# Performance work log

Measured on AMD Instinct MI355X. Metric: run time of the kernel, lower is better.

## Reference

```python
import jax, jax.numpy as jnp
import numpy as np

N_NODES = 100000
N_EDGES = 1600000
IN_F, H1, H2, H3, H4, H5, H6, NC = 512, 512, 256, 64, 64, 64, 64, 40


def _linear_params(key, fan_in, fan_out):
    k1, k2 = jax.random.split(key)
    bound = 1.0 / np.sqrt(fan_in)
    W = jax.random.uniform(k1, (fan_in, fan_out), minval=-bound, maxval=bound, dtype=jnp.float32)
    b = jax.random.uniform(k2, (fan_out,), minval=-bound, maxval=bound, dtype=jnp.float32)
    return W, b


def setup_inputs() -> dict:
    key = jax.random.key(0)
    ks = jax.random.split(key, 10)
    x = jax.random.normal(ks[0], (N_NODES, IN_F), dtype=jnp.float32)
    src = jax.random.randint(ks[1], (N_EDGES,), 0, N_NODES, dtype=jnp.int32)
    dst = jax.random.randint(ks[2], (N_EDGES,), 0, N_NODES, dtype=jnp.int32)
    W1, b1 = _linear_params(ks[3], IN_F, H1)
    W2, b2 = _linear_params(ks[4], H1, H2)
    W3, b3 = _linear_params(ks[5], H2, H3)
    Wg1, bg1 = _linear_params(ks[6], H3, H4)
    Wg2, bg2 = _linear_params(ks[7], H4, H5)
    Wg3, bg3 = _linear_params(ks[8], H5, H6)
    Wg4, bg4 = _linear_params(ks[9], H6, NC)
    return {"x": x, "src": src, "dst": dst,
            "W1": W1, "b1": b1, "W2": W2, "b2": b2, "W3": W3, "b3": b3,
            "Wg1": Wg1, "bg1": bg1, "Wg2": Wg2, "bg2": bg2,
            "Wg3": Wg3, "bg3": bg3, "Wg4": Wg4, "bg4": bg4}


def _graph_conv(h, src, dst, norm_src, norm_dst, W, b):
    # DGL GraphConv, norm='both': D_dst^{-1/2} A D_src^{-1/2} H W + b
    msg = (h * norm_src[:, None])[src]            # [E, d] gather from source nodes
    agg = jax.ops.segment_sum(msg, dst, num_segments=N_NODES)  # scatter-add to dst
    agg = agg * norm_dst[:, None]
    return agg @ W + b


def reference(x, src, dst, W1, b1, W2, b2, W3, b3,
              Wg1, bg1, Wg2, bg2, Wg3, bg3, Wg4, bg4):
    ones = jnp.ones((N_EDGES,), dtype=jnp.float32)
    deg_out = jax.ops.segment_sum(ones, src, num_segments=N_NODES)
    deg_in = jax.ops.segment_sum(ones, dst, num_segments=N_NODES)
    norm_src = jax.lax.rsqrt(jnp.clip(deg_out, 1.0))
    norm_dst = jax.lax.rsqrt(jnp.clip(deg_in, 1.0))

    h = jax.nn.relu(x @ W1 + b1)
    h = jax.nn.relu(h @ W2 + b2)
    h = jax.nn.relu(h @ W3 + b3)
    h = jax.nn.relu(_graph_conv(h, src, dst, norm_src, norm_dst, Wg1, bg1))
    h = jax.nn.relu(_graph_conv(h, src, dst, norm_src, norm_dst, Wg2, bg2))
    h = jax.nn.relu(_graph_conv(h, src, dst, norm_src, norm_dst, Wg3, bg3))
    h = jax.nn.relu(_graph_conv(h, src, dst, norm_src, norm_dst, Wg4, bg4))
    return h
```

## Files before the change

kernel.cpp:

```cpp
#include <hip/hip_runtime.h>

#define N_NODES 100000
#define N_EDGES 1600000
#define M_PAD   100096
#define BCAP    64
#define X_REAL 51200000L
#define X_PAD  ((long)M_PAD*512)

typedef __bf16 bf16x8 __attribute__((ext_vector_type(8)));
typedef float  f32x4  __attribute__((ext_vector_type(4)));
typedef unsigned short u16x8 __attribute__((ext_vector_type(8)));

__device__ __forceinline__ unsigned short f2bf(float f) {
  union { float f; unsigned u; } x; x.f = f;
  unsigned r = (x.u + 0x7FFFu + ((x.u >> 16) & 1u)) >> 16;
  return (unsigned short)r;
}

__device__ __forceinline__ void async_copy16(const void* g, void* l) {
  __builtin_amdgcn_global_load_lds((__attribute__((address_space(1))) void*)g,
                                   (__attribute__((address_space(3))) void*)l,
                                   16, 0, 0);
}


__global__ void cvt_x_kernel(const float* __restrict__ x, unsigned short* __restrict__ xb) {
  long e = ((long)blockIdx.x * 256 + threadIdx.x) * 8;
  u16x8 o;
  if (e < X_REAL) {
    float4 f0 = *(const float4*)(x + e);
    float4 f1 = *(const float4*)(x + e + 4);
    o[0] = f2bf(f0.x); o[1] = f2bf(f0.y); o[2] = f2bf(f0.z); o[3] = f2bf(f0.w);
    o[4] = f2bf(f1.x); o[5] = f2bf(f1.y); o[6] = f2bf(f1.z); o[7] = f2bf(f1.w);
  } else {
    o = (u16x8)0;
  }
  *(u16x8*)(xb + e) = o;
}

__global__ void cvt_wt_kernel(const float* __restrict__ W, unsigned short* __restrict__ Wt,
                              int K, int N, int Npad) {
  int idx = blockIdx.x * 256 + threadIdx.x;
  if (idx >= Npad * K) return;
  int n = idx / K, k = idx % K;
  Wt[idx] = (n < N) ? f2bf(W[(long)k * N + n]) : (unsigned short)0;
}

__global__ void norms_kernel(const int* __restrict__ hist,
                             float* __restrict__ nsrc, float* __restrict__ ndst) {
  int i = blockIdx.x * 256 + threadIdx.x;
  if (i >= M_PAD) return;
  if (i < N_NODES) {
    nsrc[i] = rsqrtf(fmaxf((float)hist[N_NODES + i], 1.f));
    ndst[i] = rsqrtf(fmaxf((float)hist[i], 1.f));
  } else {
    nsrc[i] = 1.f;
  }
}

template <int BM, int BN, int BK, int EPI, bool EDGES>
__launch_bounds__(256)
__global__ void gemm_bt(const unsigned short* __restrict__ A,
                        const unsigned short* __restrict__ Bt,
                        const float* __restrict__ bias,
                        const float* __restrict__ rowscale,
                        void* __restrict__ C, int K, int Nfull,
                        const int* __restrict__ esrc, const int* __restrict__ edst,
                        int* __restrict__ hist, int* __restrict__ bucket) {
  if constexpr (EDGES) {
    if (blockIdx.x == gridDim.x - 1) {
      const int stride = gridDim.y * 256;
      for (int e = blockIdx.y * 256 + threadIdx.x; e < N_EDGES; e += stride) {
        int s = esrc[e], d = edst[e];
        atomicAdd(&hist[N_NODES + s], 1);
        int p = atomicAdd(&hist[d], 1);
        if (p < BCAP) bucket[(size_t)d * BCAP + p] = s;
      }
      return;
    }
  }
  constexpr int WM = BM / 2, WN = BN / 2;
  constexpr int MI = WM / 16, NI = WN / 16;
  __shared__ __align__(16) unsigned short As[BM * BK];
  __shared__ __align__(16) unsigned short Bs[BN * BK];
  const int tid = threadIdx.x;
  const int wave = tid >> 6, lane = tid & 63;
  const int wm0 = (wave >> 1) * WM, wn0 = (wave & 1) * WN;
  const long rowBase = (long)blockIdx.y * BM;
  const int colBase = blockIdx.x * BN;
  const unsigned short* Ab = A + rowBase * K;
  const unsigned short* Bb = Bt + (long)colBase * K;
  f32x4 acc[MI][NI] = {};
  constexpr int ACH = BM * BK / 8;
  constexpr int BCH = BN * BK / 8;
  for (int k0 = 0; k0 < K; k0 += BK) {
#pragma unroll
    for (int c = tid; c < ACH; c += 256) {
      int r = (c * 8) / BK, cc = (c * 8) % BK;
      async_copy16(Ab + (long)r * K + k0 + cc, &As[c * 8]);
    }
#pragma unroll
    for (int c = tid; c < BCH; c += 256) {
      int r = (c * 8) / BK, cc = (c * 8) % BK;
      async_copy16(Bb + (long)r * K + k0 + cc, &Bs[c * 8]);
    }
    __syncthreads();
#pragma unroll
    for (int kk = 0; kk < BK; kk += 32) {
      bf16x8 af[MI], bfr[NI];
#pragma unroll
      for (int mi = 0; mi < MI; ++mi)
        af[mi] = *(const bf16x8*)&As[(wm0 + mi * 16 + (lane & 15)) * BK + kk + (lane >> 4) * 8];
#pragma unroll
      for (int ni = 0; ni < NI; ++ni)
        bfr[ni] = *(const bf16x8*)&Bs[(wn0 + ni * 16 + (lane & 15)) * BK + kk + (lane >> 4) * 8];
#pragma unroll
      for (int mi = 0; mi < MI; ++mi)
#pragma unroll
        for (int ni = 0; ni < NI; ++ni)
          acc[mi][ni] = __builtin_amdgcn_mfma_f32_16x16x32_bf16(af[mi], bfr[ni], acc[mi][ni], 0, 0, 0);
    }
    __syncthreads();
  }
  const int q = lane >> 4, c15 = lane & 15;
#pragma unroll
  for (int mi = 0; mi < MI; ++mi) {
#pragma unroll
    for (int ni = 0; ni < NI; ++ni) {
#pragma unroll
      for (int r = 0; r < 4; ++r) {
        long row = rowBase + wm0 + mi * 16 + q * 4 + r;
        int col = colBase + wn0 + ni * 16 + c15;
        float v = acc[mi][ni][r];
        if (EPI == 0) {
          v = fmaxf(v + bias[col], 0.f);
          ((unsigned short*)C)[row * Nfull + col] = f2bf(v);
        } else if (EPI == 1) {
          v = fmaxf(v + bias[col], 0.f) * rowscale[row];
          ((unsigned short*)C)[row * Nfull + col] = f2bf(v);
        } else {
          ((float*)C)[row * Nfull + col] = v;
        }
      }
    }
  }
}

template <int FINAL>
__global__ void aggregate_kernel(const float* __restrict__ t,
                                 const int* __restrict__ bucket, const int* __restrict__ cnt,
                                 const float* __restrict__ ndst, const float* __restrict__ nsrc,
                                 const float* __restrict__ bias,
                                 unsigned short* __restrict__ gout, float* __restrict__ dout) {
  int node = blockIdx.x * 4 + (threadIdx.x >> 6);
  int lane = threadIdx.x & 63;
  int r = lane >> 4;
  int c = (lane & 15) * 4;
  int n = min(cnt[node], BCAP);
  const int* bk = bucket + (size_t)node * BCAP;
  float4 acc = make_float4(0.f, 0.f, 0.f, 0.f);
  for (int i = r; i < n; i += 4) {
    int s = bk[i];
    float4 v = *(const float4*)(t + (size_t)s * 64 + c);
    acc.x += v.x; acc.y += v.y; acc.z += v.z; acc.w += v.w;
  }
  acc.x += __shfl_xor(acc.x, 16); acc.y += __shfl_xor(acc.y, 16);
  acc.z += __shfl_xor(acc.z, 16); acc.w += __shfl_xor(acc.w, 16);
  acc.x += __shfl_xor(acc.x, 32); acc.y += __shfl_xor(acc.y, 32);
  acc.z += __shfl_xor(acc.z, 32); acc.w += __shfl_xor(acc.w, 32);
  if (r == 0) {
    float nd = ndst[node];
    float v0 = fmaxf(nd * acc.x + bias[c + 0], 0.f);
    float v1 = fmaxf(nd * acc.y + bias[c + 1], 0.f);
    float v2 = fmaxf(nd * acc.z + bias[c + 2], 0.f);
    float v3 = fmaxf(nd * acc.w + bias[c + 3], 0.f);
    if (FINAL) {
      if (c < 40) {
        float* o = dout + (size_t)node * 40;
        o[c + 0] = v0; o[c + 1] = v1; o[c + 2] = v2; o[c + 3] = v3;
      }
    } else {
      float ns = nsrc[node];
      ushort4 o;
      o.x = f2bf(v0 * ns); o.y = f2bf(v1 * ns);
      o.z = f2bf(v2 * ns); o.w = f2bf(v3 * ns);
      *(ushort4*)(gout + (size_t)node * 64 + c) = o;
    }
  }
}


extern "C" void kernel_launch(void* const* d_in, const int* in_sizes, int n_in,
                              void* d_out, int out_size, void* d_ws, size_t ws_size,
                              hipStream_t stream) {
  (void)in_sizes; (void)n_in; (void)out_size; (void)ws_size;
  const float* x   = (const float*)d_in[0];
  const int* esrc  = (const int*)d_in[1];
  const int* edst  = (const int*)d_in[2];
  const float* W1  = (const float*)d_in[3];  const float* b1  = (const float*)d_in[4];
  const float* W2  = (const float*)d_in[5];  const float* b2  = (const float*)d_in[6];
  const float* W3  = (const float*)d_in[7];  const float* b3  = (const float*)d_in[8];
  const float* Wg1 = (const float*)d_in[9];  const float* bg1 = (const float*)d_in[10];
  const float* Wg2 = (const float*)d_in[11]; const float* bg2 = (const float*)d_in[12];
  const float* Wg3 = (const float*)d_in[13]; const float* bg3 = (const float*)d_in[14];
  const float* Wg4 = (const float*)d_in[15]; const float* bg4 = (const float*)d_in[16];
  float* out = (float*)d_out;

  char* ws = (char*)d_ws;
  size_t off = 0;
  auto alloc = [&](size_t bytes) -> void* {
    void* p = ws + off;
    off += (bytes + 255) & ~(size_t)255;
    return p;
  };

  unsigned short* xb = (unsigned short*)alloc((size_t)M_PAD * 512 * 2);
  unsigned short* h1 = (unsigned short*)alloc((size_t)M_PAD * 512 * 2);
  int*   bucket  = (int*)alloc((size_t)N_NODES * BCAP * 4);
  int*   hist    = (int*)alloc((size_t)2 * N_NODES * 4);
  float* nsrc    = (float*)alloc((size_t)M_PAD * 4);
  float* ndst    = (float*)alloc((size_t)N_NODES * 4);
  unsigned short* W1t  = (unsigned short*)alloc(512 * 512 * 2);
  unsigned short* W2t  = (unsigned short*)alloc(256 * 512 * 2);
  unsigned short* W3t  = (unsigned short*)alloc(64 * 256 * 2);
  unsigned short* Wg1t = (unsigned short*)alloc(64 * 64 * 2);
  unsigned short* Wg2t = (unsigned short*)alloc(64 * 64 * 2);
  unsigned short* Wg3t = (unsigned short*)alloc(64 * 64 * 2);
  unsigned short* Wg4t = (unsigned short*)alloc(64 * 64 * 2);

  unsigned short* h2 = xb;
  unsigned short* ga = (unsigned short*)((char*)xb + (size_t)M_PAD * 256 * 2);
  unsigned short* ab = (unsigned short*)((char*)ga + (size_t)M_PAD * 64 * 2);
  float*          tb = (float*)((char*)ab + (size_t)M_PAD * 64 * 2);

  hipMemsetAsync(hist, 0, (size_t)2 * N_NODES * 4, stream);

  cvt_x_kernel<<<(int)(X_PAD / 8 / 256), 256, 0, stream>>>(x, xb);

  cvt_wt_kernel<<<(512 * 512 + 255) / 256, 256, 0, stream>>>(W1, W1t, 512, 512, 512);
  cvt_wt_kernel<<<(256 * 512 + 255) / 256, 256, 0, stream>>>(W2, W2t, 512, 256, 256);
  cvt_wt_kernel<<<(64 * 256 + 255) / 256, 256, 0, stream>>>(W3, W3t, 256, 64, 64);
  cvt_wt_kernel<<<(64 * 64 + 255) / 256, 256, 0, stream>>>(Wg1, Wg1t, 64, 64, 64);
  cvt_wt_kernel<<<(64 * 64 + 255) / 256, 256, 0, stream>>>(Wg2, Wg2t, 64, 64, 64);
  cvt_wt_kernel<<<(64 * 64 + 255) / 256, 256, 0, stream>>>(Wg3, Wg3t, 64, 64, 64);
  cvt_wt_kernel<<<(64 * 64 + 255) / 256, 256, 0, stream>>>(Wg4, Wg4t, 64, 40, 64);

  const int GY = M_PAD / 128;

  gemm_bt<128, 128, 64, 0, true><<<dim3(5, GY), 256, 0, stream>>>(
      xb, W1t, b1, nullptr, h1, 512, 512, esrc, edst, hist, bucket);

  norms_kernel<<<(M_PAD + 255) / 256, 256, 0, stream>>>(hist, nsrc, ndst);

  gemm_bt<128, 128, 64, 0, false><<<dim3(2, GY), 256, 0, stream>>>(
      h1, W2t, b2, nullptr, h2, 512, 256, nullptr, nullptr, nullptr, nullptr);
  gemm_bt<128, 64, 64, 1, false><<<dim3(1, GY), 256, 0, stream>>>(
      h2, W3t, b3, nsrc, ga, 256, 64, nullptr, nullptr, nullptr, nullptr);

  gemm_bt<128, 64, 64, 2, false><<<dim3(1, GY), 256, 0, stream>>>(
      ga, Wg1t, nullptr, nullptr, tb, 64, 64, nullptr, nullptr, nullptr, nullptr);
  aggregate_kernel<0><<<N_NODES / 4, 256, 0, stream>>>(tb, bucket, hist, ndst, nsrc, bg1, ab, nullptr);

  gemm_bt<128, 64, 64, 2, false><<<dim3(1, GY), 256, 0, stream>>>(
      ab, Wg2t, nullptr, nullptr, tb, 64, 64, nullptr, nullptr, nullptr, nullptr);
  aggregate_kernel<0><<<N_NODES / 4, 256, 0, stream>>>(tb, bucket, hist, ndst, nsrc, bg2, ga, nullptr);

  gemm_bt<128, 64, 64, 2, false><<<dim3(1, GY), 256, 0, stream>>>(
      ga, Wg3t, nullptr, nullptr, tb, 64, 64, nullptr, nullptr, nullptr, nullptr);
  aggregate_kernel<0><<<N_NODES / 4, 256, 0, stream>>>(tb, bucket, hist, ndst, nsrc, bg3, ab, nullptr);

  gemm_bt<128, 64, 64, 2, false><<<dim3(1, GY), 256, 0, stream>>>(
      ab, Wg4t, nullptr, nullptr, tb, 64, 64, nullptr, nullptr, nullptr, nullptr);
  aggregate_kernel<1><<<N_NODES / 4, 256, 0, stream>>>(tb, bucket, hist, ndst, nsrc, bg4, nullptr, out);
}
```

Measured before the change: 895.9 us.

## Fuse GCN aggregation with weight GEMM and split edge bucketing across two GEMMs

Reorders each graph conv to aggregate first (A·H) and then multiply by W inside a single kernel. The bf16 aggregate is kept in LDS as a hi/lo split against a duplicated weight, which preserves precision. This removes the fp32 intermediate round-trip and halves gather bytes by reading bf16 rows instead of fp32. Edge histogram/bucketing work is also split between the W1 and W2 GEMM launches to balance the extra block. The risk is lower occupancy: the large LDS tile is 48KB and 128 nodes per block are aggregated serially per wave.

```diff
diff --git a/kernel.cpp b/kernel.cpp
--- a/kernel.cpp
+++ b/kernel.cpp
@@ -4,6 +4,7 @@
 #define N_EDGES 1600000
 #define M_PAD   100096
 #define BCAP    64
+#define E_SPLIT 1000000
 #define X_REAL 51200000L
 #define X_PAD  ((long)M_PAD*512)
 
@@ -15,6 +16,11 @@
   union { float f; unsigned u; } x; x.f = f;
   unsigned r = (x.u + 0x7FFFu + ((x.u >> 16) & 1u)) >> 16;
   return (unsigned short)r;
+}
+
+__device__ __forceinline__ float bf2f(unsigned short h) {
+  union { unsigned u; float f; } x; x.u = ((unsigned)h) << 16;
+  return x.f;
 }
 
 __device__ __forceinline__ void async_copy16(const void* g, void* l) {
@@ -46,6 +52,14 @@
   Wt[idx] = (n < N) ? f2bf(W[(long)k * N + n]) : (unsigned short)0;
 }
 
+__global__ void cvt_wt_dup_kernel(const float* __restrict__ W, unsigned short* __restrict__ Wt,
+                                  int N) {
+  int idx = blockIdx.x * 256 + threadIdx.x;
+  if (idx >= 64 * 128) return;
+  int n = idx >> 7, k = idx & 127;
+  Wt[idx] = (n < N) ? f2bf(W[(long)(k & 63) * N + n]) : (unsigned short)0;
+}
+
 __global__ void norms_kernel(const int* __restrict__ hist,
                              float* __restrict__ nsrc, float* __restrict__ ndst) {
   int i = blockIdx.x * 256 + threadIdx.x;
@@ -66,11 +80,12 @@
                         const float* __restrict__ rowscale,
                         void* __restrict__ C, int K, int Nfull,
                         const int* __restrict__ esrc, const int* __restrict__ edst,
+                        int eBeg, int eEnd,
                         int* __restrict__ hist, int* __restrict__ bucket) {
   if constexpr (EDGES) {
     if (blockIdx.x == gridDim.x - 1) {
       const int stride = gridDim.y * 256;
-      for (int e = blockIdx.y * 256 + threadIdx.x; e < N_EDGES; e += stride) {
+      for (int e = eBeg + blockIdx.y * 256 + threadIdx.x; e < eEnd; e += stride) {
         int s = esrc[e], d = edst[e];
         atomicAdd(&hist[N_NODES + s], 1);
         int p = atomicAdd(&hist[d], 1);
@@ -135,11 +150,9 @@
         if (EPI == 0) {
           v = fmaxf(v + bias[col], 0.f);
           ((unsigned short*)C)[row * Nfull + col] = f2bf(v);
-        } else if (EPI == 1) {
+        } else {
           v = fmaxf(v + bias[col], 0.f) * rowscale[row];
           ((unsigned short*)C)[row * Nfull + col] = f2bf(v);
-        } else {
-          ((float*)C)[row * Nfull + col] = v;
         }
       }
     }
@@ -147,44 +160,98 @@
 }
 
 template <int FINAL>
-__global__ void aggregate_kernel(const float* __restrict__ t,
-                                 const int* __restrict__ bucket, const int* __restrict__ cnt,
-                                 const float* __restrict__ ndst, const float* __restrict__ nsrc,
-                                 const float* __restrict__ bias,
-                                 unsigned short* __restrict__ gout, float* __restrict__ dout) {
-  int node = blockIdx.x * 4 + (threadIdx.x >> 6);
-  int lane = threadIdx.x & 63;
-  int r = lane >> 4;
-  int c = (lane & 15) * 4;
-  int n = min(cnt[node], BCAP);
-  const int* bk = bucket + (size_t)node * BCAP;
-  float4 acc = make_float4(0.f, 0.f, 0.f, 0.f);
-  for (int i = r; i < n; i += 4) {
-    int s = bk[i];
-    float4 v = *(const float4*)(t + (size_t)s * 64 + c);
-    acc.x += v.x; acc.y += v.y; acc.z += v.z; acc.w += v.w;
-  }
-  acc.x += __shfl_xor(acc.x, 16); acc.y += __shfl_xor(acc.y, 16);
-  acc.z += __shfl_xor(acc.z, 16); acc.w += __shfl_xor(acc.w, 16);
-  acc.x += __shfl_xor(acc.x, 32); acc.y += __shfl_xor(acc.y, 32);
-  acc.z += __shfl_xor(acc.z, 32); acc.w += __shfl_xor(acc.w, 32);
-  if (r == 0) {
-    float nd = ndst[node];
-    float v0 = fmaxf(nd * acc.x + bias[c + 0], 0.f);
-    float v1 = fmaxf(nd * acc.y + bias[c + 1], 0.f);
-    float v2 = fmaxf(nd * acc.z + bias[c + 2], 0.f);
-    float v3 = fmaxf(nd * acc.w + bias[c + 3], 0.f);
-    if (FINAL) {
-      if (c < 40) {
-        float* o = dout + (size_t)node * 40;
-        o[c + 0] = v0; o[c + 1] = v1; o[c + 2] = v2; o[c + 3] = v3;
+__launch_bounds__(256)
+__global__ void gcn_layer(const unsigned short* __restrict__ u,
+                          const unsigned short* __restrict__ Wt,
+                          const int* __restrict__ bucket, const int* __restrict__ cnt,
+                          const float* __restrict__ ndst, const float* __restrict__ nsrc,
+                          const float* __restrict__ bias,
+                          unsigned short* __restrict__ uout, float* __restrict__ dout) {
+  __shared__ __align__(16) unsigned short As[128 * 128];
+  __shared__ __align__(16) unsigned short Bs[64 * 128];
+  const int tid = threadIdx.x;
+  const int wave = tid >> 6, lane = tid & 63;
+  const int nodeBase = blockIdx.x * 128;
+
+#pragma unroll
+  for (int c = tid; c < 64 * 128 / 8; c += 256)
+    async_copy16(Wt + c * 8, &Bs[c * 8]);
+
+  const int r8 = lane >> 3;
+  const int c8 = (lane & 7) * 8;
+  for (int j = 0; j < 32; ++j) {
+    const int row_l = wave * 32 + j;
+    const int node = nodeBase + row_l;
+    float a0 = 0.f, a1 = 0.f, a2 = 0.f, a3 = 0.f, a4 = 0.f, a5 = 0.f, a6 = 0.f, a7 = 0.f;
+    int n = 0;
+    if (node < N_NODES) n = min(cnt[node], BCAP);
+    const int* bk = bucket + (size_t)node * BCAP;
+#pragma unroll 2
+    for (int i = r8; i < n; i += 8) {
+      int s = bk[i];
+      u16x8 v = *(const u16x8*)(u + (size_t)s * 64 + c8);
+      a0 += bf2f(v[0]); a1 += bf2f(v[1]); a2 += bf2f(v[2]); a3 += bf2f(v[3]);
+      a4 += bf2f(v[4]); a5 += bf2f(v[5]); a6 += bf2f(v[6]); a7 += bf2f(v[7]);
+    }
+#pragma unroll
+    for (int m = 8; m <= 32; m <<= 1) {
+      a0 += __shfl_xor(a0, m); a1 += __shfl_xor(a1, m);
+      a2 += __shfl_xor(a2, m); a3 += __shfl_xor(a3, m);
+      a4 += __shfl_xor(a4, m); a5 += __shfl_xor(a5, m);
+      a6 += __shfl_xor(a6, m); a7 += __shfl_xor(a7, m);
+    }
+    if (r8 == 0) {
+      float nd = (node < N_NODES) ? ndst[node] : 0.f;
+      float vv[8] = {nd * a0, nd * a1, nd * a2, nd * a3, nd * a4, nd * a5, nd * a6, nd * a7};
+      u16x8 H, L;
+#pragma unroll
+      for (int t = 0; t < 8; ++t) {
+        unsigned short h = f2bf(vv[t]);
+        H[t] = h;
+        L[t] = f2bf(vv[t] - bf2f(h));
       }
-    } else {
-      float ns = nsrc[node];
-      ushort4 o;
-      o.x = f2bf(v0 * ns); o.y = f2bf(v1 * ns);
-      o.z = f2bf(v2 * ns); o.w = f2bf(v3 * ns);
-      *(ushort4*)(gout + (size_t)node * 64 + c) = o;
+      *(u16x8*)&As[row_l * 128 + c8] = H;
+      *(u16x8*)&As[row_l * 128 + 64 + c8] = L;
+    }
+  }
+  __syncthreads();
+
+  const int wm0 = (wave >> 1) * 64, wn0 = (wave & 1) * 32;
+  f32x4 acc[4][2] = {};
+#pragma unroll
+  for (int kk = 0; kk < 128; kk += 32) {
+    bf16x8 af[4], bfr[2];
+#pragma unroll
+    for (int mi = 0; mi < 4; ++mi)
+      af[mi] = *(const bf16x8*)&As[(wm0 + mi * 16 + (lane & 15)) * 128 + kk + (lane >> 4) * 8];
+#pragma unroll
+    for (int ni = 0; ni < 2; ++ni)
+      bfr[ni] = *(const bf16x8*)&Bs[(wn0 + ni * 16 + (lane & 15)) * 128 + kk + (lane >> 4) * 8];
+#pragma unroll
+    for (int mi = 0; mi < 4; ++mi)
+#pragma unroll
+      for (int ni = 0; ni < 2; ++ni)
+        acc[mi][ni] = __builtin_amdgcn_mfma_f32_16x16x32_bf16(af[mi], bfr[ni], acc[mi][ni], 0, 0, 0);
+  }
+
+  const int q = lane >> 4, c15 = lane & 15;
+#pragma unroll
+  for (int mi = 0; mi < 4; ++mi) {
+#pragma unroll
+    for (int ni = 0; ni < 2; ++ni) {
+#pragma unroll
+      for (int r = 0; r < 4; ++r) {
+        int row = nodeBase + wm0 + mi * 16 + q * 4 + r;
+        int col = wn0 + ni * 16 + c15;
+        float bv = (FINAL && col >= 40) ? 0.f : bias[col];
+        float v = fmaxf(acc[mi][ni][r] + bv, 0.f);
+        if constexpr (FINAL) {
+          if (row < N_NODES && col < 40)
+            dout[(size_t)row * 40 + col] = v;
+        } else {
+          uout[(size_t)row * 64 + col] = f2bf(v * nsrc[row]);
+        }
+      }
     }
   }
 }
@@ -223,15 +290,14 @@
   unsigned short* W1t  = (unsigned short*)alloc(512 * 512 * 2);
   unsigned short* W2t  = (unsigned short*)alloc(256 * 512 * 2);
   unsigned short* W3t  = (unsigned short*)alloc(64 * 256 * 2);
-  unsigned short* Wg1t = (unsigned short*)alloc(64 * 64 * 2);
-  unsigned short* Wg2t = (unsigned short*)alloc(64 * 64 * 2);
-  unsigned short* Wg3t = (unsigned short*)alloc(64 * 64 * 2);
-  unsigned short* Wg4t = (unsigned short*)alloc(64 * 64 * 2);
+  unsigned short* Wg1t = (unsigned short*)alloc(64 * 128 * 2);
+  unsigned short* Wg2t = (unsigned short*)alloc(64 * 128 * 2);
+  unsigned short* Wg3t = (unsigned short*)alloc(64 * 128 * 2);
+  unsigned short* Wg4t = (unsigned short*)alloc(64 * 128 * 2);
 
   unsigned short* h2 = xb;
-  unsigned short* ga = (unsigned short*)((char*)xb + (size_t)M_PAD * 256 * 2);
-  unsigned short* ab = (unsigned short*)((char*)ga + (size_t)M_PAD * 64 * 2);
-  float*          tb = (float*)((char*)ab + (size_t)M_PAD * 64 * 2);
+  unsigned short* U0 = (unsigned short*)((char*)xb + (size_t)M_PAD * 256 * 2);
+  unsigned short* U1 = (unsigned short*)((char*)U0 + (size_t)M_PAD * 64 * 2);
 
   hipMemsetAsync(hist, 0, (size_t)2 * N_NODES * 4, stream);
 
@@ -240,36 +306,26 @@
   cvt_wt_kernel<<<(512 * 512 + 255) / 256, 256, 0, stream>>>(W1, W1t, 512, 512, 512);
   cvt_wt_kernel<<<(256 * 512 + 255) / 256, 256, 0, stream>>>(W2, W2t, 512, 256, 256);
   cvt_wt_kernel<<<(64 * 256 + 255) / 256, 256, 0, stream>>>(W3, W3t, 256, 64, 64);
-  cvt_wt_kernel<<<(64 * 64 + 255) / 256, 256, 0, stream>>>(Wg1, Wg1t, 64, 64, 64);
-  cvt_wt_kernel<<<(64 * 64 + 255) / 256, 256, 0, stream>>>(Wg2, Wg2t, 64, 64, 64);
-  cvt_wt_kernel<<<(64 * 64 + 255) / 256, 256, 0, stream>>>(Wg3, Wg3t, 64, 64, 64);
-  cvt_wt_kernel<<<(64 * 64 + 255) / 256, 256, 0, stream>>>(Wg4, Wg4t, 64, 40, 64);
+  cvt_wt_dup_kernel<<<(64 * 128 + 255) / 256, 256, 0, stream>>>(Wg1, Wg1t, 64);
+  cvt_wt_dup_kernel<<<(64 * 128 + 255) / 256, 256, 0, stream>>>(Wg2, Wg2t, 64);
+  cvt_wt_dup_kernel<<<(64 * 128 + 255) / 256, 256, 0, stream>>>(Wg3, Wg3t, 64);
+  cvt_wt_dup_kernel<<<(64 * 128 + 255) / 256, 256, 0, stream>>>(Wg4, Wg4t, 40);
 
   const int GY = M_PAD / 128;
 
   gemm_bt<128, 128, 64, 0, true><<<dim3(5, GY), 256, 0, stream>>>(
-      xb, W1t, b1, nullptr, h1, 512, 512, esrc, edst, hist, bucket);
+      xb, W1t, b1, nullptr, h1, 512, 512, esrc, edst, 0, E_SPLIT, hist, bucket);
+
+  gemm_bt<128, 128, 64, 0, true><<<dim3(3, GY), 256, 0, stream>>>(
+      h1, W2t, b2, nullptr, h2, 512, 256, esrc, edst, E_SPLIT, N_EDGES, hist, bucket);
 
   norms_kernel<<<(M_PAD + 255) / 256, 256, 0, stream>>>(hist, nsrc, ndst);
 
-  gemm_bt<128, 128, 64, 0, false><<<dim3(2, GY), 256, 0, stream>>>(
-      h1, W2t, b2, nullptr, h2, 512, 256, nullptr, nullptr, nullptr, nullptr);
   gemm_bt<128, 64, 64, 1, false><<<dim3(1, GY), 256, 0, stream>>>(
-      h2, W3t, b3, nsrc, ga, 256, 64, nullptr, nullptr, nullptr, nullptr);
-
-  gemm_bt<128, 64, 64, 2, false><<<dim3(1, GY), 256, 0, stream>>>(
-      ga, Wg1t, nullptr, nullptr, tb, 64, 64, nullptr, nullptr, nullptr, nullptr);
-  aggregate_kernel<0><<<N_NODES / 4, 256, 0, stream>>>(tb, bucket, hist, ndst, nsrc, bg1, ab, nullptr);
-
-  gemm_bt<128, 64, 64, 2, false><<<dim3(1, GY), 256, 0, stream>>>(
-      ab, Wg2t, nullptr, nullptr, tb, 64, 64, nullptr, nullptr, nullptr, nullptr);
-  aggregate_kernel<0><<<N_NODES / 4, 256, 0, stream>>>(tb, bucket, hist, ndst, nsrc, bg2, ga, nullptr);
-
-  gemm_bt<128, 64, 64, 2, false><<<dim3(1, GY), 256, 0, stream>>>(
-      ga, Wg3t, nullptr, nullptr, tb, 64, 64, nullptr, nullptr, nullptr, nullptr);
-  aggregate_kernel<0><<<N_NODES / 4, 256, 0, stream>>>(tb, bucket, hist, ndst, nsrc, bg3, ab, nullptr);
-
-  gemm_bt<128, 64, 64, 2, false><<<dim3(1, GY), 256, 0, stream>>>(
-      ab, Wg4t, nullptr, nullptr, tb, 64, 64, nullptr, nullptr, nullptr, nullptr);
-  aggregate_kernel<1><<<N_NODES / 4, 256, 0, stream>>>(tb, bucket, hist, ndst, nsrc, bg4, nullptr, out);
-}
+      h2, W3t, b3, nsrc, U0, 256, 64, nullptr, nullptr, 0, 0, nullptr, nullptr);
+
+  gcn_layer<0><<<GY, 256, 0, stream>>>(U0, Wg1t, bucket, hist, ndst, nsrc, bg1, U1, nullptr);
+  gcn_layer<0><<<GY, 256, 0, stream>>>(U1, Wg2t, bucket, hist, ndst, nsrc, bg2, U0, nullptr);
+  gcn_layer<0><<<GY, 256, 0, stream>>>(U0, Wg3t, bucket, hist, ndst, nsrc, bg3, U1, nullptr);
+  gcn_layer<1><<<GY, 256, 0, stream>>>(U1, Wg4t, bucket, hist, ndst, nsrc, bg4, nullptr, out);
+}
```

New measurement: 1.141 ms. 27.3% more time.
